# Performance work log

Measured on AMD Instinct MI355X. Metric: run time of the kernel, lower is better.

Reference implementation:

```python
import jax, jax.numpy as jnp
import numpy as np

B, S, H, I, E = 4, 2048, 768, 3072, 8
TOP_K = 2
ALPHA_BALANCE = 0.01
ENERGY_ALPHA = 0.0


def setup_inputs() -> dict:
    key = jax.random.key(0)
    ks = jax.random.split(key, 5)
    g = lambda k, shape: jax.random.normal(k, shape, jnp.float32) * 0.02
    return {
        "hidden_states": jax.random.normal(ks[0], (B, S, H), jnp.float32),
        "router_w": g(ks[1], (H, E)),
        "router_b": jnp.zeros((E,), jnp.float32),
        "w1": g(ks[2], (E, H, I)),
        "b1": jnp.zeros((E, I), jnp.float32),
        "w2": g(ks[3], (E, I, H)),
        "b2": jnp.zeros((E, H), jnp.float32),
    }


def reference(hidden_states, router_w, router_b, w1, b1, w2, b2):
    # --- routing: top-2 softmax gate scattered back to dense [B,S,E] ---
    router_logits = hidden_states @ router_w + router_b          # [B,S,E]
    top_v, top_i = jax.lax.top_k(router_logits, TOP_K)           # [B,S,2]
    top_w = jax.nn.softmax(top_v, axis=-1)                       # [B,S,2]
    gating = jnp.sum(
        jax.nn.one_hot(top_i, E, dtype=router_logits.dtype) * top_w[..., None],
        axis=-2,
    )                                                            # [B,S,E]

    # --- aux losses (torch .std() is unbiased, ddof=1) ---
    importance = gating.sum(axis=(0, 1))                         # [E]
    mean_imp = importance.mean()
    load_balancing_loss = ALPHA_BALANCE * (
        jnp.var(importance, ddof=1) / (mean_imp ** 2 + 1e-8)
    )
    probs_mean = gating.mean(axis=(0, 1))                        # [E]
    energy_loss = ENERGY_ALPHA * jnp.sum(probs_mean ** 2)
    aux_loss = load_balancing_loss + energy_loss

    # --- dense all-expert FFN (faithful to the naive original) ---
    # h: [B,S,E,I]; exact (erf) GELU matches torch nn.GELU default
    h = jax.nn.gelu(
        jnp.einsum("bsh,ehf->bsef", hidden_states, w1) + b1,
        approximate=False,
    )
    expert_outputs = jnp.einsum("bsef,efh->bseh", h, w2) + b2    # [B,S,E,H]
    # dropout is identity in eval mode

    # --- weighted combine (the bmm in the original) ---
    final_output = jnp.einsum("bse,bseh->bsh", gating, expert_outputs)
    return final_output, aux_loss, gating
```

## Files before the change

### kernel.cpp

```cpp
#include <hip/hip_runtime.h>
#include <math.h>

#define NB 4
#define NS 2048
#define HD 768
#define ID 3072
#define NE 8
#define NTOK (NB*NS)
#define NPAIR (NTOK*2)

#define BMF 128
#define BNF 256
#define BKF 64
#define MAXTF 136
#define KS2 24

#define BMS 32
#define KCH 128
#define NCHUNK (ID/KCH)
#define MAXTS (NPAIR/BMS + NE)
#define LDP 36

typedef unsigned short u16;
typedef __attribute__((ext_vector_type(8))) short bf16x8;
typedef __attribute__((ext_vector_type(4))) float f32x4;

__device__ __forceinline__ float bf2f(u16 u) {
  union { unsigned int i; float f; } v; v.i = ((unsigned int)u) << 16; return v.f;
}
__device__ __forceinline__ u16 f2bf(float f) {
  union { float fl; unsigned int i; } v; v.fl = f;
  unsigned int r = v.i + 0x7fffu + ((v.i >> 16) & 1u);
  return (u16)(r >> 16);
}
__device__ __forceinline__ void gload16(const void* g, void* l) {
  __builtin_amdgcn_global_load_lds(
      (const __attribute__((address_space(1))) void*)g,
      (__attribute__((address_space(3))) void*)l, 16, 0, 0);
}
__device__ __forceinline__ float gelu_fast(float x) {
  float u = 0.7978845608028654f * (x + 0.044715f * x * x * x);
  float e = __expf(2.f * u);
  float t = 1.f - 2.f / (e + 1.f);
  return 0.5f * x * (1.f + t);
}
__device__ __forceinline__ int xcd_swz_2d() {
  int nwg  = gridDim.x * gridDim.y;
  int orig = blockIdx.x + blockIdx.y * gridDim.x;
  int q = nwg >> 3, r = nwg & 7;
  int xcd = orig & 7, i = orig >> 3;
  return (xcd < r) ? (xcd * (q + 1) + i) : (r * (q + 1) + (xcd - r) * q + i);
}

__global__ __launch_bounds__(256) void router_kernel(
    const float* __restrict__ x, const float* __restrict__ rw,
    const float* __restrict__ rb, float* __restrict__ gating,
    int* __restrict__ topi, float* __restrict__ topw)
{
  int wid = threadIdx.x >> 6, lane = threadIdx.x & 63;
  int tok = blockIdx.x * 4 + wid;
  float acc[NE];
  #pragma unroll
  for (int e = 0; e < NE; ++e) acc[e] = 0.f;
  const float* xr = x + (size_t)tok * HD;
  #pragma unroll
  for (int r = 0; r < 3; ++r) {
    int h4 = (r*64 + lane) * 4;
    float4 xv = *(const float4*)&xr[h4];
    const float4* wr = (const float4*)(rw + (size_t)h4 * NE);
    float4 a0 = wr[0], c0 = wr[1], a1 = wr[2], c1 = wr[3];
    float4 a2 = wr[4], c2 = wr[5], a3 = wr[6], c3 = wr[7];
    acc[0] += xv.x*a0.x + xv.y*a1.x + xv.z*a2.x + xv.w*a3.x;
    acc[1] += xv.x*a0.y + xv.y*a1.y + xv.z*a2.y + xv.w*a3.y;
    acc[2] += xv.x*a0.z + xv.y*a1.z + xv.z*a2.z + xv.w*a3.z;
    acc[3] += xv.x*a0.w + xv.y*a1.w + xv.z*a2.w + xv.w*a3.w;
    acc[4] += xv.x*c0.x + xv.y*c1.x + xv.z*c2.x + xv.w*c3.x;
    acc[5] += xv.x*c0.y + xv.y*c1.y + xv.z*c2.y + xv.w*c3.y;
    acc[6] += xv.x*c0.z + xv.y*c1.z + xv.z*c2.z + xv.w*c3.z;
    acc[7] += xv.x*c0.w + xv.y*c1.w + xv.z*c2.w + xv.w*c3.w;
  }
  #pragma unroll
  for (int off = 1; off < 64; off <<= 1) {
    #pragma unroll
    for (int e = 0; e < NE; ++e) acc[e] += __shfl_xor(acc[e], off);
  }
  float lg[NE];
  #pragma unroll
  for (int e = 0; e < NE; ++e) lg[e] = acc[e] + rb[e];
  int i0 = 0;
  #pragma unroll
  for (int e = 1; e < NE; ++e) if (lg[e] > lg[i0]) i0 = e;
  int i1 = (i0 == 0) ? 1 : 0;
  #pragma unroll
  for (int e = 0; e < NE; ++e) if (e != i0 && lg[e] > lg[i1]) i1 = e;
  float ex = expf(lg[i1] - lg[i0]);
  float s = 1.f + ex;
  float w0 = 1.f / s, w1v = ex / s;
  if (lane < NE)
    gating[(size_t)tok*NE + lane] = (lane==i0) ? w0 : (lane==i1 ? w1v : 0.f);
  if (lane == 0) {
    topi[2*tok] = i0; topi[2*tok+1] = i1;
    topw[2*tok] = w0; topw[2*tok+1] = w1v;
  }
}

__global__ __launch_bounds__(1024) void plan_kernel(
    const int* __restrict__ topi, const float* __restrict__ topw,
    int* __restrict__ offs, int* __restrict__ tilesc,
    int* __restrict__ ptok, float* __restrict__ pwv, int bm,
    float* __restrict__ aux)
{
  __shared__ int   wcnt[16][NE];
  __shared__ int   wbase[16][NE];
  __shared__ float wsum[16][NE];
  int tid = threadIdx.x, w = tid >> 6, lane = tid & 63;
  int base = w * 1024;

  int cnt[NE];
  #pragma unroll
  for (int e = 0; e < NE; ++e) cnt[e] = 0;
  #pragma unroll
  for (int it = 0; it < 16; ++it) {
    int ti = topi[base + it*64 + lane];
    #pragma unroll
    for (int e = 0; e < NE; ++e) {
      unsigned long long m = __ballot(ti == e);
      cnt[e] += __popcll(m);
    }
  }
  if (lane == 0)
    #pragma unroll
    for (int e = 0; e < NE; ++e) wcnt[w][e] = cnt[e];
  __syncthreads();

  if (tid == 0) {
    int o = 0, tt = 0;
    for (int e = 0; e < NE; ++e) {
      offs[e] = o; tilesc[e] = tt;
      int run = o, tot = 0;
      for (int ww = 0; ww < 16; ++ww) { wbase[ww][e] = run; run += wcnt[ww][e]; tot += wcnt[ww][e]; }
      o += tot;
      tt += (tot + bm - 1) / bm;
    }
    offs[NE] = o; tilesc[NE] = tt;
  }
  __syncthreads();

  int run[NE];
  float lsum[NE];
  #pragma unroll
  for (int e = 0; e < NE; ++e) { run[e] = wbase[w][e]; lsum[e] = 0.f; }
  unsigned long long lt = (1ull << lane) - 1ull;
  #pragma unroll
  for (int it = 0; it < 16; ++it) {
    int p = base + it*64 + lane;
    int ti = topi[p];
    float tw = topw[p];
    int idx = 0;
    #pragma unroll
    for (int e = 0; e < NE; ++e) {
      unsigned long long m = __ballot(ti == e);
      int r = run[e] + __popcll(m & lt);
      if (ti == e) idx = r;
      run[e] += __popcll(m);
      lsum[e] += (ti == e) ? tw : 0.f;
    }
    ptok[idx] = p >> 1;
    pwv[idx] = tw;
  }
  #pragma unroll
  for (int off = 1; off < 64; off <<= 1) {
    #pragma unroll
    for (int e = 0; e < NE; ++e) lsum[e] += __shfl_xor(lsum[e], off);
  }
  if (lane == 0)
    #pragma unroll
    for (int e = 0; e < NE; ++e) wsum[w][e] = lsum[e];
  __syncthreads();
  if (tid == 0) {
    float imp[NE];
    for (int e = 0; e < NE; ++e) {
      float s = 0.f;
      for (int ww = 0; ww < 16; ++ww) s += wsum[ww][e];
      imp[e] = s;
    }
    float mean = 0.f;
    for (int e = 0; e < NE; ++e) mean += imp[e];
    mean *= (1.f/NE);
    float var = 0.f;
    for (int e = 0; e < NE; ++e) { float d = imp[e] - mean; var += d*d; }
    var *= (1.f/(NE-1));
    aux[0] = 0.01f * var / (mean*mean + 1e-8f);
  }
}

__global__ __launch_bounds__(256) void cvt_x_kernel(
    const float* __restrict__ x, u16* __restrict__ xb)
{
  int i = (blockIdx.x * 256 + threadIdx.x) * 8;
  float4 a = *(const float4*)&x[i];
  float4 b = *(const float4*)&x[i + 4];
  uint4 o;
  o.x = (unsigned)f2bf(a.x) | ((unsigned)f2bf(a.y) << 16);
  o.y = (unsigned)f2bf(a.z) | ((unsigned)f2bf(a.w) << 16);
  o.z = (unsigned)f2bf(b.x) | ((unsigned)f2bf(b.y) << 16);
  o.w = (unsigned)f2bf(b.z) | ((unsigned)f2bf(b.w) << 16);
  *(uint4*)&xb[i] = o;
}

__global__ __launch_bounds__(256) void transpose_bf16_kernel(
    const float* __restrict__ src, u16* __restrict__ dst, int R, int C)
{
  __shared__ u16 tile[64][65];
  int e = blockIdx.z;
  const float* s = src + (size_t)e * R * C;
  u16* d = dst + (size_t)e * R * C;
  int c0 = blockIdx.x * 64, r0 = blockIdx.y * 64;
  int t = threadIdx.x;
  int rr = t >> 4, c4 = (t & 15) * 4;
  #pragma unroll
  for (int rep = 0; rep < 4; ++rep) {
    int r = rr + rep * 16;
    float4 v = *(const float4*)&s[(size_t)(r0 + r) * C + c0 + c4];
    tile[r][c4+0] = f2bf(v.x); tile[r][c4+1] = f2bf(v.y);
    tile[r][c4+2] = f2bf(v.z); tile[r][c4+3] = f2bf(v.w);
  }
  __syncthreads();
  #pragma unroll
  for (int rep = 0; rep < 4; ++rep) {
    int w = t + rep * 256;
    int c = w >> 4, rq = (w & 15) * 4;
    ushort4 o;
    o.x = tile[rq+0][c]; o.y = tile[rq+1][c];
    o.z = tile[rq+2][c]; o.w = tile[rq+3][c];
    *(ushort4*)&d[(size_t)(c0 + c) * R + r0 + rq] = o;
  }
}

__global__ __launch_bounds__(512, 2) void moe_gemm1_kernel(
    const u16* __restrict__ xbf, const u16* __restrict__ w1t,
    const float* __restrict__ b1, const int* __restrict__ offs,
    const int* __restrict__ tilesc, const int* __restrict__ ptok,
    const float* __restrict__ pwv, u16* __restrict__ hbuf, int t0)
{
  __shared__ __align__(16) u16 As[BMF*BKF];
  __shared__ __align__(16) u16 Bs[BNF*BKF];
  __shared__ int   toks_s[BMF];
  __shared__ float gws_s[BMF];

  int wkid = xcd_swz_2d();
  int tile = wkid % gridDim.x;
  int n0   = (wkid / gridDim.x) * BNF;

  int t = t0 + tile;
  if (t >= tilesc[NE]) return;
  int e = 0;
  #pragma unroll
  for (int k = 1; k < NE; ++k) if (t >= tilesc[k]) e = k;
  int row0 = offs[e] + (t - tilesc[e]) * BMF;
  int nrows = offs[e+1] - row0; if (nrows > BMF) nrows = BMF;
  int tid = threadIdx.x, wid = tid >> 6, lane = tid & 63;

  if (tid < BMF) {
    int tk = -1; float g = 0.f;
    if (tid < nrows) { tk = ptok[row0 + tid]; g = pwv[row0 + tid]; }
    toks_s[tid] = tk; gws_s[tid] = g;
  }
  __syncthreads();

  int ssub = tid >> 3;
  int sbc  = (tid & 7) << 4;
  int swz  = sbc ^ ((ssub & 7) << 4);
  int tkA0 = toks_s[ssub];      if (tkA0 < 0) tkA0 = 0;
  int tkA1 = toks_s[64 + ssub]; if (tkA1 < 0) tkA1 = 0;
  const char* aS0 = (const char*)xbf + (size_t)tkA0 * (HD*2) + swz;
  const char* aS1 = (const char*)xbf + (size_t)tkA1 * (HD*2) + swz;
  const char* bS0 = (const char*)w1t + ((size_t)e*ID + n0 +       ssub) * (HD*2) + swz;
  const char* bS1 = (const char*)w1t + ((size_t)e*ID + n0 +  64 + ssub) * (HD*2) + swz;
  const char* bS2 = (const char*)w1t + ((size_t)e*ID + n0 + 128 + ssub) * (HD*2) + swz;
  const char* bS3 = (const char*)w1t + ((size_t)e*ID + n0 + 192 + ssub) * (HD*2) + swz;
  u16* aD0 = As + wid*512;
  u16* aD1 = As + 4096 + wid*512;
  u16* bD0 = Bs + wid*512;
  u16* bD1 = Bs +  4096 + wid*512;
  u16* bD2 = Bs +  8192 + wid*512;
  u16* bD3 = Bs + 12288 + wid*512;

  int wr = wid >> 2, wc = wid & 3;
  int lr = lane & 15, lg = lane >> 4;

  f32x4 acc[4][4];
  #pragma unroll
  for (int m = 0; m < 4; ++m)
    #pragma unroll
    for (int n = 0; n < 4; ++n) { f32x4 z = {0.f,0.f,0.f,0.f}; acc[m][n] = z; }

  for (int ks = 0; ks < HD/BKF; ++ks) {
    __syncthreads();
    int ko = ks * 128;
    gload16(aS0 + ko, aD0);
    gload16(aS1 + ko, aD1);
    gload16(bS0 + ko, bD0);
    gload16(bS1 + ko, bD1);
    gload16(bS2 + ko, bD2);
    gload16(bS3 + ko, bD3);
    __syncthreads();
    #pragma unroll
    for (int k2 = 0; k2 < 2; ++k2) {
      bf16x8 af[4], bfr[4];
      #pragma unroll
      for (int m = 0; m < 4; ++m) {
        int row = wr*64 + m*16 + lr;
        int bo = (k2*64 + lg*16) ^ ((row & 7) << 4);
        af[m] = *(const bf16x8*)((const char*)As + row*128 + bo);
      }
      #pragma unroll
      for (int n = 0; n < 4; ++n) {
        int row = wc*64 + n*16 + lr;
        int bo = (k2*64 + lg*16) ^ ((row & 7) << 4);
        bfr[n] = *(const bf16x8*)((const char*)Bs + row*128 + bo);
      }
      #pragma unroll
      for (int m = 0; m < 4; ++m)
        #pragma unroll
        for (int n = 0; n < 4; ++n)
          acc[m][n] = __builtin_amdgcn_mfma_f32_16x16x32_bf16(af[m], bfr[n], acc[m][n], 0, 0, 0);
    }
  }

  int rbase = wr*64, cbase = n0 + wc*64;
  const float* b1e = b1 + (size_t)e * ID;
  float b1v[4];
  #pragma unroll
  for (int n = 0; n < 4; ++n) b1v[n] = b1e[cbase + n*16 + lr];
  size_t hrow0 = (size_t)tile * BMF;
  #pragma unroll
  for (int m = 0; m < 4; ++m) {
    #pragma unroll
    for (int j = 0; j < 4; ++j) {
      int row = rbase + m*16 + lg*4 + j;
      float g = gws_s[row];
      u16* hp = hbuf + (hrow0 + row) * ID + cbase + lr;
      #pragma unroll
      for (int n = 0; n < 4; ++n) {
        float v = acc[m][n][j] + b1v[n];
        hp[n*16] = f2bf(gelu_fast(v) * g);
      }
    }
  }
}

__global__ __launch_bounds__(512, 2) void moe_gemm2_kernel(
    const u16* __restrict__ hbuf, const u16* __restrict__ w2t,
    const float* __restrict__ b2, const int* __restrict__ offs,
    const int* __restrict__ tilesc, const int* __restrict__ ptok,
    const float* __restrict__ pwv, float* __restrict__ out, int t0)
{
  __shared__ __align__(16) u16 As[BMF*BKF];
  __shared__ __align__(16) u16 Bs[BNF*BKF];
  __shared__ int   toks_s[BMF];
  __shared__ float gws_s[BMF];

  int wkid = xcd_swz_2d();
  int tile = wkid % gridDim.x;
  int n0   = (wkid / gridDim.x) * BNF;
  int z    = blockIdx.z;
  int kbase = z * KS2 * 128;

  int t = t0 + tile;
  if (t >= tilesc[NE]) return;
  int e = 0;
  #pragma unroll
  for (int k = 1; k < NE; ++k) if (t >= tilesc[k]) e = k;
  int row0 = offs[e] + (t - tilesc[e]) * BMF;
  int nrows = offs[e+1] - row0; if (nrows > BMF) nrows = BMF;
  int tid = threadIdx.x, wid = tid >> 6, lane = tid & 63;

  if (tid < BMF) {
    int tk = -1; float g = 0.f;
    if (tid < nrows) { tk = ptok[row0 + tid]; g = pwv[row0 + tid]; }
    toks_s[tid] = tk; gws_s[tid] = g;
  }
  __syncthreads();

  int ssub = tid >> 3;
  int sbc  = (tid & 7) << 4;
  int swz  = sbc ^ ((ssub & 7) << 4);
  const char* aS0 = (const char*)hbuf + ((size_t)tile*BMF +       ssub) * (ID*2) + swz + kbase;
  const char* aS1 = (const char*)hbuf + ((size_t)tile*BMF +  64 + ssub) * (ID*2) + swz + kbase;
  const char* bS0 = (const char*)w2t + ((size_t)e*HD + n0 +       ssub) * (ID*2) + swz + kbase;
  const char* bS1 = (const char*)w2t + ((size_t)e*HD + n0 +  64 + ssub) * (ID*2) + swz + kbase;
  const char* bS2 = (const char*)w2t + ((size_t)e*HD + n0 + 128 + ssub) * (ID*2) + swz + kbase;
  const char* bS3 = (const char*)w2t + ((size_t)e*HD + n0 + 192 + ssub) * (ID*2) + swz + kbase;
  u16* aD0 = As + wid*512;
  u16* aD1 = As + 4096 + wid*512;
  u16* bD0 = Bs + wid*512;
  u16* bD1 = Bs +  4096 + wid*512;
  u16* bD2 = Bs +  8192 + wid*512;
  u16* bD3 = Bs + 12288 + wid*512;

  int wr = wid >> 2, wc = wid & 3;
  int lr = lane & 15, lg = lane >> 4;

  f32x4 acc[4][4];
  #pragma unroll
  for (int m = 0; m < 4; ++m)
    #pragma unroll
    for (int n = 0; n < 4; ++n) { f32x4 zz = {0.f,0.f,0.f,0.f}; acc[m][n] = zz; }

  for (int ks = 0; ks < KS2; ++ks) {
    __syncthreads();
    int ko = ks * 128;
    gload16(aS0 + ko, aD0);
    gload16(aS1 + ko, aD1);
    gload16(bS0 + ko, bD0);
    gload16(bS1 + ko, bD1);
    gload16(bS2 + ko, bD2);
    gload16(bS3 + ko, bD3);
    __syncthreads();
    #pragma unroll
    for (int k2 = 0; k2 < 2; ++k2) {
      bf16x8 af[4], bfr[4];
      #pragma unroll
      for (int m = 0; m < 4; ++m) {
        int row = wr*64 + m*16 + lr;
        int bo = (k2*64 + lg*16) ^ ((row & 7) << 4);
        af[m] = *(const bf16x8*)((const char*)As + row*128 + bo);
      }
      #pragma unroll
      for (int n = 0; n < 4; ++n) {
        int row = wc*64 + n*16 + lr;
        int bo = (k2*64 + lg*16) ^ ((row & 7) << 4);
        bfr[n] = *(const bf16x8*)((const char*)Bs + row*128 + bo);
      }
      #pragma unroll
      for (int m = 0; m < 4; ++m)
        #pragma unroll
        for (int n = 0; n < 4; ++n)
          acc[m][n] = __builtin_amdgcn_mfma_f32_16x16x32_bf16(af[m], bfr[n], acc[m][n], 0, 0, 0);
    }
  }

  int rbase = wr*64, cbase = n0 + wc*64;
  const float* b2e = b2 + (size_t)e * HD;
  float b2v[4];
  #pragma unroll
  for (int n = 0; n < 4; ++n) b2v[n] = (z == 0) ? b2e[cbase + n*16 + lr] : 0.f;
  #pragma unroll
  for (int m = 0; m < 4; ++m) {
    #pragma unroll
    for (int j = 0; j < 4; ++j) {
      int row = rbase + m*16 + lg*4 + j;
      int tk = toks_s[row];
      if (tk < 0) continue;
      float g = gws_s[row];
      float* op = out + (size_t)tk * HD + cbase + lr;
      #pragma unroll
      for (int n = 0; n < 4; ++n)
        atomicAdd(&op[n*16], acc[m][n][j] + g * b2v[n]);
    }
  }
}

__global__ __launch_bounds__(512, 4) void ffn_kernel(
    const float* __restrict__ x, const float* __restrict__ w1,
    const float* __restrict__ b1, const float* __restrict__ w2,
    const float* __restrict__ b2, const int* __restrict__ offs,
    const int* __restrict__ tilesc, const int* __restrict__ ptok,
    const float* __restrict__ pwv, float* __restrict__ out)
{
  __shared__ u16 x_t[HD][LDP];
  __shared__ u16 h_t[KCH][LDP];
  __shared__ int   toks[BMS];
  __shared__ float gws[BMS];

  int bid = blockIdx.x;
  if (bid >= tilesc[NE]) return;
  int e = 0;
  #pragma unroll
  for (int k = 1; k < NE; ++k) if (bid >= tilesc[k]) e = k;
  int tile = bid - tilesc[e];
  int row0 = offs[e] + tile * BMS;
  int nrows = offs[e+1] - row0;
  if (nrows > BMS) nrows = BMS;

  int tid = threadIdx.x;
  if (tid < BMS) {
    int tk = -1; float g = 0.f;
    if (tid < nrows) { tk = ptok[row0 + tid]; g = pwv[row0 + tid]; }
    toks[tid] = tk; gws[tid] = g;
  }
  __syncthreads();

  for (int idx = tid; idx < BMS*HD; idx += 512) {
    int m = idx / HD, h = idx - m*HD;
    int tk = toks[m];
    x_t[h][m] = (tk >= 0) ? f2bf(x[(size_t)tk*HD + h]) : (u16)0;
  }

  int w4 = (tid >> 6) << 2;
  int lane = tid & 63;
  const float* w1e = w1 + (size_t)e * HD * ID;
  const float* w2e = w2 + (size_t)e * ID * HD;
  const float* b1e = b1 + (size_t)e * ID;
  const float* b2e = b2 + (size_t)e * HD;

  float acc[4][12];
  #pragma unroll
  for (int jm = 0; jm < 4; ++jm)
    #pragma unroll
    for (int jn = 0; jn < 12; ++jn) acc[jm][jn] = 0.f;

  __syncthreads();
  float gwr[4];
  #pragma unroll
  for (int jm = 0; jm < 4; ++jm) gwr[jm] = gws[w4 + jm];

  for (int c = 0; c < NCHUNK; ++c) {
    int i0 = c * KCH;
    float hb[4][2];
    #pragma unroll
    for (int jm = 0; jm < 4; ++jm) { hb[jm][0] = 0.f; hb[jm][1] = 0.f; }
    const float* p = w1e + i0 + lane;
    #pragma unroll 4
    for (int h = 0; h < HD; ++h) {
      ushort4 xu = *(const ushort4*)&x_t[h][w4];
      float wv0 = p[0];
      float wv1 = p[64];
      p += ID;
      float x0 = bf2f(xu.x), x1 = bf2f(xu.y), x2 = bf2f(xu.z), x3 = bf2f(xu.w);
      hb[0][0] += x0*wv0; hb[1][0] += x1*wv0; hb[2][0] += x2*wv0; hb[3][0] += x3*wv0;
      hb[0][1] += x0*wv1; hb[1][1] += x1*wv1; hb[2][1] += x2*wv1; hb[3][1] += x3*wv1;
    }
    float b1v0 = b1e[i0 + lane];
    float b1v1 = b1e[i0 + 64 + lane];
    __syncthreads();
    #pragma unroll
    for (int q = 0; q < 2; ++q) {
      int il = lane + 64*q;
      float bv = q ? b1v1 : b1v0;
      #pragma unroll
      for (int jm = 0; jm < 4; ++jm) {
        float v = hb[jm][q] + bv;
        v = 0.5f * v * (1.f + erff(v * 0.70710678118654752f));
        h_t[il][w4 + jm] = f2bf(v * gwr[jm]);
      }
    }
    __syncthreads();
    const float* q2 = w2e + (size_t)i0 * HD + lane;
    for (int k = 0; k < KCH; ++k) {
      ushort4 hu = *(const ushort4*)&h_t[k][w4];
      float h0 = bf2f(hu.x), h1 = bf2f(hu.y), h2 = bf2f(hu.z), h3 = bf2f(hu.w);
      #pragma unroll
      for (int jn = 0; jn < 12; ++jn) {
        float wv = q2[64*jn];
        acc[0][jn] += h0*wv; acc[1][jn] += h1*wv;
        acc[2][jn] += h2*wv; acc[3][jn] += h3*wv;
      }
      q2 += HD;
    }
  }

  #pragma unroll
  for (int jm = 0; jm < 4; ++jm) {
    int m = w4 + jm;
    int tk = toks[m];
    if (tk < 0) continue;
    float g = gwr[jm];
    float* orow = out + (size_t)tk * HD;
    #pragma unroll
    for (int jn = 0; jn < 12; ++jn) {
      int n = lane + 64*jn;
      atomicAdd(&orow[n], acc[jm][jn] + g * b2e[n]);
    }
  }
}

extern "C" void kernel_launch(void* const* d_in, const int* in_sizes, int n_in,
                              void* d_out, int out_size, void* d_ws, size_t ws_size,
                              hipStream_t stream)
{
  const float* x  = (const float*)d_in[0];
  const float* rw = (const float*)d_in[1];
  const float* rb = (const float*)d_in[2];
  const float* w1 = (const float*)d_in[3];
  const float* b1 = (const float*)d_in[4];
  const float* w2 = (const float*)d_in[5];
  const float* b2 = (const float*)d_in[6];

  float* out    = (float*)d_out;
  float* aux    = out + (size_t)NTOK * HD;
  float* gating = aux + 1;

  int*   W  = (int*)d_ws;
  float* Wf = (float*)d_ws;
  int*   offs   = W + 16;
  int*   tilesc = W + 32;
  int*   topi   = W + 64;
  float* topw   = Wf + 64 + NPAIR;
  int*   ptok   = W + 64 + 2*NPAIR;
  float* pwv    = Wf + 64 + 3*NPAIR;
  char*  wsB    = (char*)d_ws;
  const size_t OFF_XBF = 262400;
  const size_t OFF_W1T = OFF_XBF + (size_t)NTOK*HD*2;
  const size_t OFF_W2T = OFF_W1T + (size_t)NE*ID*HD*2;
  const size_t OFF_H   = OFF_W2T + (size_t)NE*ID*HD*2;
  const size_t NEED_FULL = OFF_H + (size_t)MAXTF*BMF*ID*2;
  const size_t NEED_2    = OFF_H + (size_t)68*BMF*ID*2;

  u16* xbf = (u16*)(wsB + OFF_XBF);
  u16* w1t = (u16*)(wsB + OFF_W1T);
  u16* w2t = (u16*)(wsB + OFF_W2T);
  u16* hb  = (u16*)(wsB + OFF_H);

  hipMemsetAsync(d_out, 0, (size_t)NTOK * HD * sizeof(float), stream);

  router_kernel<<<NTOK/4, 256, 0, stream>>>(x, rw, rb, gating, topi, topw);

  if (ws_size >= NEED_2) {
    plan_kernel<<<1, 1024, 0, stream>>>(topi, topw, offs, tilesc, ptok, pwv, BMF, aux);
    cvt_x_kernel<<<(NTOK*HD)/(8*256), 256, 0, stream>>>(x, xbf);
    transpose_bf16_kernel<<<dim3(ID/64, HD/64, NE), 256, 0, stream>>>(w1, w1t, HD, ID);
    transpose_bf16_kernel<<<dim3(HD/64, ID/64, NE), 256, 0, stream>>>(w2, w2t, ID, HD);
    int cht = (ws_size >= NEED_FULL) ? MAXTF : 68;
    int nch = (ws_size >= NEED_FULL) ? 1 : 2;
    for (int c = 0; c < nch; ++c) {
      moe_gemm1_kernel<<<dim3(cht, ID/BNF), 512, 0, stream>>>(
          xbf, w1t, b1, offs, tilesc, ptok, pwv, hb, c*cht);
      moe_gemm2_kernel<<<dim3(cht, HD/BNF, 2), 512, 0, stream>>>(
          hb, w2t, b2, offs, tilesc, ptok, pwv, out, c*cht);
    }
  } else {
    plan_kernel<<<1, 1024, 0, stream>>>(topi, topw, offs, tilesc, ptok, pwv, BMS, aux);
    ffn_kernel<<<MAXTS, 512, 0, stream>>>(x, w1, b1, w2, b2, offs, tilesc, ptok, pwv, out);
  }
}
```

Baseline: 368.0 us.

## Halve gemm1 grid with two N-tiles per block, drop gemm2 split-K

GEMM1 now has each block loop over two 256-wide N tiles, which halves the grid in N. GEMM2 drops its 2-way split-K over the intermediate dimension and runs the full K loop per block, so there are half as many atomicAdds to the output. The chunked fallback for smaller workspaces is removed, so the MFMA path now needs the full workspace. The intent is lower atomic traffic and launch/tail overhead. The cost is fewer blocks in flight (136x6 and 136x3), which may underfill the GPU and lengthen the serial K loop in GEMM2.

After: 412.1 us. 12.0% more time.

```diff
diff --git a/kernel.cpp b/kernel.cpp
--- a/kernel.cpp
+++ b/kernel.cpp
@@ -13,7 +13,6 @@
 #define BNF 256
 #define BKF 64
 #define MAXTF 136
-#define KS2 24
 
 #define BMS 32
 #define KCH 128
@@ -250,7 +249,7 @@
 
   int wkid = xcd_swz_2d();
   int tile = wkid % gridDim.x;
-  int n0   = (wkid / gridDim.x) * BNF;
+  int nc2  = wkid / gridDim.x;
 
   int t = t0 + tile;
   if (t >= tilesc[NE]) return;
@@ -275,10 +274,6 @@
   int tkA1 = toks_s[64 + ssub]; if (tkA1 < 0) tkA1 = 0;
   const char* aS0 = (const char*)xbf + (size_t)tkA0 * (HD*2) + swz;
   const char* aS1 = (const char*)xbf + (size_t)tkA1 * (HD*2) + swz;
-  const char* bS0 = (const char*)w1t + ((size_t)e*ID + n0 +       ssub) * (HD*2) + swz;
-  const char* bS1 = (const char*)w1t + ((size_t)e*ID + n0 +  64 + ssub) * (HD*2) + swz;
-  const char* bS2 = (const char*)w1t + ((size_t)e*ID + n0 + 128 + ssub) * (HD*2) + swz;
-  const char* bS3 = (const char*)w1t + ((size_t)e*ID + n0 + 192 + ssub) * (HD*2) + swz;
   u16* aD0 = As + wid*512;
   u16* aD1 = As + 4096 + wid*512;
   u16* bD0 = Bs + wid*512;
@@ -288,14 +283,134 @@
 
   int wr = wid >> 2, wc = wid & 3;
   int lr = lane & 15, lg = lane >> 4;
+  size_t hrow0 = (size_t)tile * BMF;
+
+  for (int nn = 0; nn < 2; ++nn) {
+    int n0 = nc2 * 512 + nn * 256;
+    const char* bS0 = (const char*)w1t + ((size_t)e*ID + n0 +       ssub) * (HD*2) + swz;
+    const char* bS1 = (const char*)w1t + ((size_t)e*ID + n0 +  64 + ssub) * (HD*2) + swz;
+    const char* bS2 = (const char*)w1t + ((size_t)e*ID + n0 + 128 + ssub) * (HD*2) + swz;
+    const char* bS3 = (const char*)w1t + ((size_t)e*ID + n0 + 192 + ssub) * (HD*2) + swz;
+
+    f32x4 acc[4][4];
+    #pragma unroll
+    for (int m = 0; m < 4; ++m)
+      #pragma unroll
+      for (int n = 0; n < 4; ++n) { f32x4 z = {0.f,0.f,0.f,0.f}; acc[m][n] = z; }
+
+    for (int ks = 0; ks < HD/BKF; ++ks) {
+      __syncthreads();
+      int ko = ks * 128;
+      gload16(aS0 + ko, aD0);
+      gload16(aS1 + ko, aD1);
+      gload16(bS0 + ko, bD0);
+      gload16(bS1 + ko, bD1);
+      gload16(bS2 + ko, bD2);
+      gload16(bS3 + ko, bD3);
+      __syncthreads();
+      #pragma unroll
+      for (int k2 = 0; k2 < 2; ++k2) {
+        bf16x8 af[4], bfr[4];
+        #pragma unroll
+        for (int m = 0; m < 4; ++m) {
+          int row = wr*64 + m*16 + lr;
+          int bo = (k2*64 + lg*16) ^ ((row & 7) << 4);
+          af[m] = *(const bf16x8*)((const char*)As + row*128 + bo);
+        }
+        #pragma unroll
+        for (int n = 0; n < 4; ++n) {
+          int row = wc*64 + n*16 + lr;
+          int bo = (k2*64 + lg*16) ^ ((row & 7) << 4);
+          bfr[n] = *(const bf16x8*)((const char*)Bs + row*128 + bo);
+        }
+        #pragma unroll
+        for (int m = 0; m < 4; ++m)
+          #pragma unroll
+          for (int n = 0; n < 4; ++n)
+            acc[m][n] = __builtin_amdgcn_mfma_f32_16x16x32_bf16(af[m], bfr[n], acc[m][n], 0, 0, 0);
+      }
+    }
+
+    int rbase = wr*64, cbase = n0 + wc*64;
+    const float* b1e = b1 + (size_t)e * ID;
+    float b1v[4];
+    #pragma unroll
+    for (int n = 0; n < 4; ++n) b1v[n] = b1e[cbase + n*16 + lr];
+    #pragma unroll
+    for (int m = 0; m < 4; ++m) {
+      #pragma unroll
+      for (int j = 0; j < 4; ++j) {
+        int row = rbase + m*16 + lg*4 + j;
+        float g = gws_s[row];
+        u16* hp = hbuf + (hrow0 + row) * ID + cbase + lr;
+        #pragma unroll
+        for (int n = 0; n < 4; ++n) {
+          float v = acc[m][n][j] + b1v[n];
+          hp[n*16] = f2bf(gelu_fast(v) * g);
+        }
+      }
+    }
+    __syncthreads();
+  }
+}
+
+__global__ __launch_bounds__(512, 2) void moe_gemm2_kernel(
+    const u16* __restrict__ hbuf, const u16* __restrict__ w2t,
+    const float* __restrict__ b2, const int* __restrict__ offs,
+    const int* __restrict__ tilesc, const int* __restrict__ ptok,
+    const float* __restrict__ pwv, float* __restrict__ out, int t0)
+{
+  __shared__ __align__(16) u16 As[BMF*BKF];
+  __shared__ __align__(16) u16 Bs[BNF*BKF];
+  __shared__ int   toks_s[BMF];
+  __shared__ float gws_s[BMF];
+
+  int wkid = xcd_swz_2d();
+  int tile = wkid % gridDim.x;
+  int n0   = (wkid / gridDim.x) * BNF;
+
+  int t = t0 + tile;
+  if (t >= tilesc[NE]) return;
+  int e = 0;
+  #pragma unroll
+  for (int k = 1; k < NE; ++k) if (t >= tilesc[k]) e = k;
+  int row0 = offs[e] + (t - tilesc[e]) * BMF;
+  int nrows = offs[e+1] - row0; if (nrows > BMF) nrows = BMF;
+  int tid = threadIdx.x, wid = tid >> 6, lane = tid & 63;
+
+  if (tid < BMF) {
+    int tk = -1; float g = 0.f;
+    if (tid < nrows) { tk = ptok[row0 + tid]; g = pwv[row0 + tid]; }
+    toks_s[tid] = tk; gws_s[tid] = g;
+  }
+  __syncthreads();
+
+  int ssub = tid >> 3;
+  int sbc  = (tid & 7) << 4;
+  int swz  = sbc ^ ((ssub & 7) << 4);
+  const char* aS0 = (const char*)hbuf + ((size_t)tile*BMF +       ssub) * (ID*2) + swz;
+  const char* aS1 = (const char*)hbuf + ((size_t)tile*BMF +  64 + ssub) * (ID*2) + swz;
+  const char* bS0 = (const char*)w2t + ((size_t)e*HD + n0 +       ssub) * (ID*2) + swz;
+  const char* bS1 = (const char*)w2t + ((size_t)e*HD + n0 +  64 + ssub) * (ID*2) + swz;
+  const char* bS2 = (const char*)w2t + ((size_t)e*HD + n0 + 128 + ssub) * (ID*2) + swz;
+  const char* bS3 = (const char*)w2t + ((size_t)e*HD + n0 + 192 + ssub) * (ID*2) + swz;
+  u16* aD0 = As + wid*512;
+  u16* aD1 = As + 4096 + wid*512;
+  u16* bD0 = Bs + wid*512;
+  u16* bD1 = Bs +  4096 + wid*512;
+  u16* bD2 = Bs +  8192 + wid*512;
+  u16* bD3 = Bs + 12288 + wid*512;
+
+  int wr = wid >> 2, wc = wid & 3;
+  int lr = lane & 15, lg = lane >> 4;
 
   f32x4 acc[4][4];
   #pragma unroll
   for (int m = 0; m < 4; ++m)
     #pragma unroll
-    for (int n = 0; n < 4; ++n) { f32x4 z = {0.f,0.f,0.f,0.f}; acc[m][n] = z; }
-
-  for (int ks = 0; ks < HD/BKF; ++ks) {
+    for (int n = 0; n < 4; ++n) { f32x4 zz = {0.f,0.f,0.f,0.f}; acc[m][n] = zz; }
+
+  for (int ks = 0; ks < ID/BKF; ++ks) {
     __syncthreads();
     int ko = ks * 128;
     gload16(aS0 + ko, aD0);
@@ -329,123 +444,10 @@
   }
 
   int rbase = wr*64, cbase = n0 + wc*64;
-  const float* b1e = b1 + (size_t)e * ID;
-  float b1v[4];
-  #pragma unroll
-  for (int n = 0; n < 4; ++n) b1v[n] = b1e[cbase + n*16 + lr];
-  size_t hrow0 = (size_t)tile * BMF;
-  #pragma unroll
-  for (int m = 0; m < 4; ++m) {
-    #pragma unroll
-    for (int j = 0; j < 4; ++j) {
-      int row = rbase + m*16 + lg*4 + j;
-      float g = gws_s[row];
-      u16* hp = hbuf + (hrow0 + row) * ID + cbase + lr;
-      #pragma unroll
-      for (int n = 0; n < 4; ++n) {
-        float v = acc[m][n][j] + b1v[n];
-        hp[n*16] = f2bf(gelu_fast(v) * g);
-      }
-    }
-  }
-}
-
-__global__ __launch_bounds__(512, 2) void moe_gemm2_kernel(
-    const u16* __restrict__ hbuf, const u16* __restrict__ w2t,
-    const float* __restrict__ b2, const int* __restrict__ offs,
-    const int* __restrict__ tilesc, const int* __restrict__ ptok,
-    const float* __restrict__ pwv, float* __restrict__ out, int t0)
-{
-  __shared__ __align__(16) u16 As[BMF*BKF];
-  __shared__ __align__(16) u16 Bs[BNF*BKF];
-  __shared__ int   toks_s[BMF];
-  __shared__ float gws_s[BMF];
-
-  int wkid = xcd_swz_2d();
-  int tile = wkid % gridDim.x;
-  int n0   = (wkid / gridDim.x) * BNF;
-  int z    = blockIdx.z;
-  int kbase = z * KS2 * 128;
-
-  int t = t0 + tile;
-  if (t >= tilesc[NE]) return;
-  int e = 0;
-  #pragma unroll
-  for (int k = 1; k < NE; ++k) if (t >= tilesc[k]) e = k;
-  int row0 = offs[e] + (t - tilesc[e]) * BMF;
-  int nrows = offs[e+1] - row0; if (nrows > BMF) nrows = BMF;
-  int tid = threadIdx.x, wid = tid >> 6, lane = tid & 63;
-
-  if (tid < BMF) {
-    int tk = -1; float g = 0.f;
-    if (tid < nrows) { tk = ptok[row0 + tid]; g = pwv[row0 + tid]; }
-    toks_s[tid] = tk; gws_s[tid] = g;
-  }
-  __syncthreads();
-
-  int ssub = tid >> 3;
-  int sbc  = (tid & 7) << 4;
-  int swz  = sbc ^ ((ssub & 7) << 4);
-  const char* aS0 = (const char*)hbuf + ((size_t)tile*BMF +       ssub) * (ID*2) + swz + kbase;
-  const char* aS1 = (const char*)hbuf + ((size_t)tile*BMF +  64 + ssub) * (ID*2) + swz + kbase;
-  const char* bS0 = (const char*)w2t + ((size_t)e*HD + n0 +       ssub) * (ID*2) + swz + kbase;
-  const char* bS1 = (const char*)w2t + ((size_t)e*HD + n0 +  64 + ssub) * (ID*2) + swz + kbase;
-  const char* bS2 = (const char*)w2t + ((size_t)e*HD + n0 + 128 + ssub) * (ID*2) + swz + kbase;
-  const char* bS3 = (const char*)w2t + ((size_t)e*HD + n0 + 192 + ssub) * (ID*2) + swz + kbase;
-  u16* aD0 = As + wid*512;
-  u16* aD1 = As + 4096 + wid*512;
-  u16* bD0 = Bs + wid*512;
-  u16* bD1 = Bs +  4096 + wid*512;
-  u16* bD2 = Bs +  8192 + wid*512;
-  u16* bD3 = Bs + 12288 + wid*512;
-
-  int wr = wid >> 2, wc = wid & 3;
-  int lr = lane & 15, lg = lane >> 4;
-
-  f32x4 acc[4][4];
-  #pragma unroll
-  for (int m = 0; m < 4; ++m)
-    #pragma unroll
-    for (int n = 0; n < 4; ++n) { f32x4 zz = {0.f,0.f,0.f,0.f}; acc[m][n] = zz; }
-
-  for (int ks = 0; ks < KS2; ++ks) {
-    __syncthreads();
-    int ko = ks * 128;
-    gload16(aS0 + ko, aD0);
-    gload16(aS1 + ko, aD1);
-    gload16(bS0 + ko, bD0);
-    gload16(bS1 + ko, bD1);
-    gload16(bS2 + ko, bD2);
-    gload16(bS3 + ko, bD3);
-    __syncthreads();
-    #pragma unroll
-    for (int k2 = 0; k2 < 2; ++k2) {
-      bf16x8 af[4], bfr[4];
-      #pragma unroll
-      for (int m = 0; m < 4; ++m) {
-        int row = wr*64 + m*16 + lr;
-        int bo = (k2*64 + lg*16) ^ ((row & 7) << 4);
-        af[m] = *(const bf16x8*)((const char*)As + row*128 + bo);
-      }
-      #pragma unroll
-      for (int n = 0; n < 4; ++n) {
-        int row = wc*64 + n*16 + lr;
-        int bo = (k2*64 + lg*16) ^ ((row & 7) << 4);
-        bfr[n] = *(const bf16x8*)((const char*)Bs + row*128 + bo);
-      }
-      #pragma unroll
-      for (int m = 0; m < 4; ++m)
-        #pragma unroll
-        for (int n = 0; n < 4; ++n)
-          acc[m][n] = __builtin_amdgcn_mfma_f32_16x16x32_bf16(af[m], bfr[n], acc[m][n], 0, 0, 0);
-    }
-  }
-
-  int rbase = wr*64, cbase = n0 + wc*64;
   const float* b2e = b2 + (size_t)e * HD;
   float b2v[4];
   #pragma unroll
-  for (int n = 0; n < 4; ++n) b2v[n] = (z == 0) ? b2e[cbase + n*16 + lr] : 0.f;
+  for (int n = 0; n < 4; ++n) b2v[n] = b2e[cbase + n*16 + lr];
   #pragma unroll
   for (int m = 0; m < 4; ++m) {
     #pragma unroll
@@ -617,19 +619,15 @@
 
   router_kernel<<<NTOK/4, 256, 0, stream>>>(x, rw, rb, gating, topi, topw);
 
-  if (ws_size >= NEED_2) {
+  if (ws_size >= NEED_FULL) {
     plan_kernel<<<1, 1024, 0, stream>>>(topi, topw, offs, tilesc, ptok, pwv, BMF, aux);
     cvt_x_kernel<<<(NTOK*HD)/(8*256), 256, 0, stream>>>(x, xbf);
     transpose_bf16_kernel<<<dim3(ID/64, HD/64, NE), 256, 0, stream>>>(w1, w1t, HD, ID);
     transpose_bf16_kernel<<<dim3(HD/64, ID/64, NE), 256, 0, stream>>>(w2, w2t, ID, HD);
-    int cht = (ws_size >= NEED_FULL) ? MAXTF : 68;
-    int nch = (ws_size >= NEED_FULL) ? 1 : 2;
-    for (int c = 0; c < nch; ++c) {
-      moe_gemm1_kernel<<<dim3(cht, ID/BNF), 512, 0, stream>>>(
-          xbf, w1t, b1, offs, tilesc, ptok, pwv, hb, c*cht);
-      moe_gemm2_kernel<<<dim3(cht, HD/BNF, 2), 512, 0, stream>>>(
-          hb, w2t, b2, offs, tilesc, ptok, pwv, out, c*cht);
-    }
+    moe_gemm1_kernel<<<dim3(MAXTF, ID/BNF/2), 512, 0, stream>>>(
+        xbf, w1t, b1, offs, tilesc, ptok, pwv, hb, 0);
+    moe_gemm2_kernel<<<dim3(MAXTF, HD/BNF), 512, 0, stream>>>(
+        hb, w2t, b2, offs, tilesc, ptok, pwv, out, 0);
   } else {
     plan_kernel<<<1, 1024, 0, stream>>>(topi, topw, offs, tilesc, ptok, pwv, BMS, aux);
     ffn_kernel<<<MAXTS, 512, 0, stream>>>(x, w1, b1, w2, b2, offs, tilesc, ptok, pwv, out);
```
